# Kernel optimization log

Measured on AMD Instinct MI355X. Metric: run time of the kernel, lower is better.

The kernel has to match this reference:

```python
import jax, jax.numpy as jnp
import numpy as np

SMOOTH = 1e-6
K = 64  # num_selection_features


def setup_inputs() -> dict:
    key = jax.random.key(0)
    kx, kw, kb = jax.random.split(key, 3)
    x = jax.random.normal(kx, (8, 256, 128, 128), dtype=jnp.float32)
    # 1x1 conv: Conv2d(K, 1) -> weight [1, K, 1, 1]; store as [K] and scalar bias
    w = jax.random.normal(kw, (K,), dtype=jnp.float32) * (1.0 / np.sqrt(K))
    b = jax.random.normal(kb, (1,), dtype=jnp.float32) * 0.01
    return {"x": x, "w": w, "b": b}


def reference(x, w, b):
    B, C, H, W = x.shape
    s = jax.nn.sigmoid(x)
    uncertainty = -s * jnp.log(s + SMOOTH)           # [B,C,H,W]
    score = jnp.mean(uncertainty, axis=(2, 3))       # [B,C]
    # topk smallest -> top_k of negated score
    _, idx = jax.lax.top_k(-score, K)                # [B,K]
    selected = jnp.take_along_axis(x, idx[:, :, None, None], axis=1)  # [B,K,H,W]
    # 1x1 conv (K->1) + sigmoid
    attn = jax.nn.sigmoid(jnp.einsum('bkhw,k->bhw', selected, w) + b[0])  # [B,H,W]
    return x * attn[:, None, :, :]
```

## Files before the change

### kernel.cpp

```cpp
#include <hip/hip_runtime.h>

constexpr int B  = 8;
constexpr int C  = 256;
constexpr int HW = 128 * 128;
constexpr int K  = 64;

__device__ __forceinline__ float uncert_rank(float v) {
    float t = __expf(-v);
    float a = 1.0f + t;
    return __log2f(a) * __builtin_amdgcn_rcpf(a);
}

__global__ __launch_bounds__(256) void score_kernel(const float* __restrict__ x,
                                                    float* __restrict__ score) {
    const int plane = blockIdx.x;
    const float4* xp = (const float4*)(x + (size_t)plane * HW);
    const int t = threadIdx.x;

    float acc = 0.0f;
#pragma unroll
    for (int i = 0; i < 16; ++i) {
        float4 v = xp[t + i * 256];
        acc += uncert_rank(v.x) + uncert_rank(v.y) + uncert_rank(v.z) + uncert_rank(v.w);
    }
#pragma unroll
    for (int off = 32; off > 0; off >>= 1) acc += __shfl_down(acc, off, 64);

    __shared__ float smem[4];
    if ((t & 63) == 0) smem[t >> 6] = acc;
    __syncthreads();
    if (t == 0) score[plane] = smem[0] + smem[1] + smem[2] + smem[3];
}

__global__ __launch_bounds__(256) void topk_kernel(const float* __restrict__ score,
                                                   int* __restrict__ sel) {
    const int b = blockIdx.x;
    const int t = threadIdx.x;
    __shared__ float sc[C];
    sc[t] = score[b * C + t];
    __syncthreads();

    const float my = sc[t];
    int rank = 0;
#pragma unroll 8
    for (int j = 0; j < C; ++j) {
        float o = sc[j];
        rank += (o < my) || (o == my && j < t);
    }
    if (rank < K) sel[b * K + rank] = t;
}

__global__ __launch_bounds__(256) void attn_mul_kernel(const float* __restrict__ x,
                                                       const int* __restrict__ sel,
                                                       const float* __restrict__ w,
                                                       const float* __restrict__ bias,
                                                       float* __restrict__ out) {
    const int b     = blockIdx.x >> 5;
    const int chunk = blockIdx.x & 31;
    const int t     = threadIdx.x;

    __shared__ float ws[K];
    __shared__ int   chs[K];
    if (t < K) { ws[t] = w[t]; chs[t] = sel[b * K + t]; }
    __syncthreads();

    const int p2 = chunk * 256 + t;
    const float2* xb = (const float2*)(x + (size_t)b * C * HW);
    float2*       ob = (float2*)(out + (size_t)b * C * HW);

    float ax = 0.f, ay = 0.f;
#pragma unroll 16
    for (int k = 0; k < K; ++k) {
        float2 v = xb[(size_t)chs[k] * (HW / 2) + p2];
        float wk = ws[k];
        ax += wk * v.x; ay += wk * v.y;
    }
    const float b0 = bias[0];
    float ea = __expf(-(ax + b0));
    float eb = __expf(-(ay + b0));
    const float sa = __builtin_amdgcn_rcpf(1.0f + ea);
    const float sb = __builtin_amdgcn_rcpf(1.0f + eb);

#pragma unroll 8
    for (int c = 0; c < C; ++c) {
        const size_t idx = (size_t)c * (HW / 2) + p2;
        float2 v = xb[idx];
        float2 o; o.x = v.x * sa; o.y = v.y * sb;
        ob[idx] = o;
    }
}

extern "C" void kernel_launch(void* const* d_in, const int* in_sizes, int n_in,
                              void* d_out, int out_size, void* d_ws, size_t ws_size,
                              hipStream_t stream) {
    const float* x    = (const float*)d_in[0];
    const float* w    = (const float*)d_in[1];
    const float* bias = (const float*)d_in[2];
    float* out = (float*)d_out;

    char* ws = (char*)d_ws;
    float* score = (float*)ws;
    int*   sel   = (int*)(ws + 8192);

    score_kernel<<<B * C, 256, 0, stream>>>(x, score);
    topk_kernel<<<B, C, 0, stream>>>(score, sel);
    attn_mul_kernel<<<B * 32, 256, 0, stream>>>(x, sel, w, bias, out);
}
```

Measured before the change: 270.5 us.

## Fuse top-k into attention kernel and reuse selected channel loads for output

Measured after the change: 261.0 us. -3.5%, faster.

```diff
diff --git a/kernel.cpp b/kernel.cpp
--- a/kernel.cpp
+++ b/kernel.cpp
@@ -32,58 +32,63 @@
     if (t == 0) score[plane] = smem[0] + smem[1] + smem[2] + smem[3];
 }
 
-__global__ __launch_bounds__(256) void topk_kernel(const float* __restrict__ score,
-                                                   int* __restrict__ sel) {
-    const int b = blockIdx.x;
-    const int t = threadIdx.x;
-    __shared__ float sc[C];
-    sc[t] = score[b * C + t];
-    __syncthreads();
-
-    const float my = sc[t];
-    int rank = 0;
-#pragma unroll 8
-    for (int j = 0; j < C; ++j) {
-        float o = sc[j];
-        rank += (o < my) || (o == my && j < t);
-    }
-    if (rank < K) sel[b * K + rank] = t;
-}
-
-__global__ __launch_bounds__(256) void attn_mul_kernel(const float* __restrict__ x,
-                                                       const int* __restrict__ sel,
-                                                       const float* __restrict__ w,
-                                                       const float* __restrict__ bias,
-                                                       float* __restrict__ out) {
+__global__ __launch_bounds__(256, 1) void attn_mul_kernel(const float* __restrict__ x,
+                                                          const float* __restrict__ score,
+                                                          const float* __restrict__ w,
+                                                          const float* __restrict__ bias,
+                                                          float* __restrict__ out) {
     const int b     = blockIdx.x >> 5;
     const int chunk = blockIdx.x & 31;
     const int t     = threadIdx.x;
 
+    __shared__ float sc[C];
     __shared__ float ws[K];
     __shared__ int   chs[K];
-    if (t < K) { ws[t] = w[t]; chs[t] = sel[b * K + t]; }
+    __shared__ int   unch[C - K];
+
+    sc[t] = score[b * C + t];
+    if (t < K) ws[t] = w[t];
+    __syncthreads();
+
+    {
+        const float my = sc[t];
+        int rank = 0;
+#pragma unroll 8
+        for (int j = 0; j < C; ++j) {
+            float o = sc[j];
+            rank += (o < my) || (o == my && j < t);
+        }
+        if (rank < K) chs[rank] = t;
+        else          unch[rank - K] = t;
+    }
     __syncthreads();
 
     const int p2 = chunk * 256 + t;
     const float2* xb = (const float2*)(x + (size_t)b * C * HW);
     float2*       ob = (float2*)(out + (size_t)b * C * HW);
 
+    float2 st[K];
     float ax = 0.f, ay = 0.f;
-#pragma unroll 16
+#pragma unroll
     for (int k = 0; k < K; ++k) {
         float2 v = xb[(size_t)chs[k] * (HW / 2) + p2];
+        st[k] = v;
         float wk = ws[k];
         ax += wk * v.x; ay += wk * v.y;
     }
     const float b0 = bias[0];
-    float ea = __expf(-(ax + b0));
-    float eb = __expf(-(ay + b0));
-    const float sa = __builtin_amdgcn_rcpf(1.0f + ea);
-    const float sb = __builtin_amdgcn_rcpf(1.0f + eb);
+    const float sa = __builtin_amdgcn_rcpf(1.0f + __expf(-(ax + b0)));
+    const float sb = __builtin_amdgcn_rcpf(1.0f + __expf(-(ay + b0)));
+
+#pragma unroll
+    for (int k = 0; k < K; ++k) {
+        float2 o; o.x = st[k].x * sa; o.y = st[k].y * sb;
+        ob[(size_t)chs[k] * (HW / 2) + p2] = o;
+    }
 
 #pragma unroll 8
-    for (int c = 0; c < C; ++c) {
-        const size_t idx = (size_t)c * (HW / 2) + p2;
+    for (int j = 0; j < C - K; ++j) {
+        const size_t idx = (size_t)unch[j] * (HW / 2) + p2;
         float2 v = xb[idx];
         float2 o; o.x = v.x * sa; o.y = v.y * sb;
         ob[idx] = o;
@@ -98,11 +103,8 @@
     const float* bias = (const float*)d_in[2];
     float* out = (float*)d_out;
 
-    char* ws = (char*)d_ws;
-    float* score = (float*)ws;
-    int*   sel   = (int*)(ws + 8192);
+    float* score = (float*)d_ws;
 
     score_kernel<<<B * C, 256, 0, stream>>>(x, score);
-    topk_kernel<<<B, C, 0, stream>>>(score, sel);
-    attn_mul_kernel<<<B * 32, 256, 0, stream>>>(x, sel, w, bias, out);
+    attn_mul_kernel<<<B * 32, 256, 0, stream>>>(x, score, w, bias, out);
 }
```
